# Performance work log

Hardware: AMD Instinct MI355X
Metric: run time of the kernel (lower is better)

The kernel has to match this reference:

```python
import jax, jax.numpy as jnp
import numpy as np

# ---- static configuration (mirrors qg_flux __init__ args) ----
F = 1600.0
MREFIN = 8
H1 = 0.25
NU1 = 2
NU2 = 2
NCYC = 2
M = 513
N = 513
DX = 0.001953125
DY = 0.001953125
R = 1.0
RKB = 1e-06
RKH = 1e-08
RKH2 = 2e-11
BATCH = 16
HS = [H1 / 2 ** (MREFIN - k - 1) for k in range(MREFIN)]  # grid spacing per level (0 = finest)


def _pad1(x):
    return jnp.pad(x, ((0, 0), (0, 0), (1, 1), (1, 1)))


def relax(psi, q, h):
    # Relax_Conv: 3x3 valid conv (cross stencil on psi, -1 center on q) scaled by 1/(4+F h^2), then zero-pad 1.
    c = 1.0 / (4.0 + F * h * h)
    inner = c * (psi[:, :, :-2, 1:-1] + psi[:, :, 2:, 1:-1]
                 + psi[:, :, 1:-1, :-2] + psi[:, :, 1:-1, 2:]
                 - q[:, :, 1:-1, 1:-1])
    return _pad1(inner)


def rescale(psi, q, h):
    # Rescal_Conv: 5x5 stride-2 valid conv, centers at odd-even input points, then zero-pad 1.
    d = 4.0 + F * h * h
    S, T = psi.shape[-2], psi.shape[-1]
    no = (S - 5) // 2 + 1
    mo = (T - 5) // 2 + 1
    rc = slice(2, 2 * no + 1, 2)   # center rows
    cc = slice(2, 2 * mo + 1, 2)   # center cols
    ctr = psi[:, :, rc, cc]
    up = psi[:, :, 1:2 * no:2, cc]
    dn = psi[:, :, 3:2 * no + 2:2, cc]
    lf = psi[:, :, rc, 1:2 * mo:2]
    rt = psi[:, :, rc, 3:2 * mo + 2:2]
    qc = q[:, :, rc, cc]
    out = 4.0 * (d * ctr - up - dn - lf - rt + qc)
    return _pad1(out)


def bilinear_up(x, hf, wf):
    # torch F.interpolate(mode='bilinear', align_corners=True)
    hc, wc = x.shape[-2], x.shape[-1]
    ys = jnp.linspace(0.0, hc - 1.0, hf)
    xs = jnp.linspace(0.0, wc - 1.0, wf)
    y0 = jnp.clip(jnp.floor(ys), 0, hc - 2).astype(jnp.int32)
    x0 = jnp.clip(jnp.floor(xs), 0, wc - 2).astype(jnp.int32)
    wy = (ys - y0)[:, None]
    wx = xs - x0
    row = x[:, :, y0, :] * (1.0 - wy) + x[:, :, y0 + 1, :] * wy
    return row[:, :, :, x0] * (1.0 - wx) + row[:, :, :, x0 + 1] * wx


def helmholtz(psiguess, q):
    bs, ch, w, h = psiguess.shape
    shapes = [(int(np.ceil(w / 2 ** k)), int(np.ceil(h / 2 ** k))) for k in range(MREFIN)]
    psis = [jnp.zeros((bs, ch) + s, dtype=psiguess.dtype) for s in shapes]
    qs = [jnp.zeros((bs, ch) + s, dtype=psiguess.dtype) for s in shapes]
    psis[0] = psiguess
    qs[0] = q * HS[0] ** 2
    for _ic in range(NCYC):
        # downsweep: relax fine->coarse, restrict residual-equation RHS
        for k in range(MREFIN):
            if k != 0:
                psis[k] = jnp.zeros_like(psis[k])
            for _ in range(NU1):
                psis[k] = relax(psis[k], qs[k], HS[k])
            if k < MREFIN - 1:
                qs[k + 1] = rescale(psis[k], qs[k], HS[k])
        # upsweep (faithful to original loop ordering, incl. its intadd indexing)
        for k in range(MREFIN):
            lvl = MREFIN - k - 1
            for _ in range(NU2):
                psis[lvl] = relax(psis[lvl], qs[lvl], HS[lvl])
            if k > 0:
                hf, wf = psis[k - 1].shape[-2], psis[k - 1].shape[-1]
                psis[k - 1] = psis[k - 1] + bilinear_up(psis[k], hf, wf)
    return psis[0]


def arakawa(A, B):
    # 9-point Arakawa Jacobian, zero on boundary
    Amm = A[:, :, :-2, :-2]; Am0 = A[:, :, :-2, 1:-1]; Amp = A[:, :, :-2, 2:]
    A0m = A[:, :, 1:-1, :-2];                         A0p = A[:, :, 1:-1, 2:]
    Apm = A[:, :, 2:, :-2];  Ap0 = A[:, :, 2:, 1:-1]; App = A[:, :, 2:, 2:]
    Bmm = B[:, :, :-2, :-2]; Bm0 = B[:, :, :-2, 1:-1]; Bmp = B[:, :, :-2, 2:]
    B0m = B[:, :, 1:-1, :-2];                          B0p = B[:, :, 1:-1, 2:]
    Bpm = B[:, :, 2:, :-2];  Bp0 = B[:, :, 2:, 1:-1];  Bpp = B[:, :, 2:, 2:]
    J = ((A0m - Am0) * Bmm
         + (Amm + A0m - Amp - A0p) * Bm0
         + (Am0 - A0p) * Bmp
         + (Apm + Ap0 - Amm - Am0) * B0m
         + (Am0 + Amp - Ap0 - App) * B0p
         + (Ap0 - A0m) * Bpm
         + (A0p + App - A0m - Apm) * Bp0
         + (A0p - Ap0) * Bpp)
    return _pad1(J / (12.0 * DX * DY))


def laplacian(A):
    dx2, dy2 = DX * DX, DY * DY
    inner = ((A[:, :, 1:-1, :-2] + A[:, :, 1:-1, 2:]) / dx2
             + (A[:, :, :-2, 1:-1] + A[:, :, 2:, 1:-1]) / dy2
             - A[:, :, 1:-1, 1:-1] * (2.0 / dx2 + 2.0 / dy2))
    return _pad1(inner)


def setup_inputs() -> dict:
    key = jax.random.key(0)
    k1, k2, k3 = jax.random.split(key, 3)
    PSIGUESS = 0.1 * jax.random.normal(k1, (BATCH, 1, M, N), dtype=jnp.float32)
    Q = 0.1 * jax.random.normal(k2, (BATCH, 1, M, N), dtype=jnp.float32)
    CURLT = 0.1 * jax.random.normal(k3, (1, M, N), dtype=jnp.float32)
    return {"t": 0, "PSIGUESS": PSIGUESS, "Q": Q, "CURLT": CURLT}


def reference(t, PSIGUESS, Q, CURLT):
    PSI = helmholtz(PSIGUESS, Q)
    J = arakawa(PSI, Q)
    Z = laplacian(PSI)
    Z2 = laplacian(Z)
    Z4 = laplacian(Z2)
    base = -R * J - RKB * Z + RKH * Z2 - RKH2 * Z4 + CURLT  # CURLT (1,M,N) broadcasts
    inner = base[:, :, 1:-1, 1:-1] - (0.5 / DX) * (PSI[:, :, 1:-1, 2:] - PSI[:, :, 1:-1, :-2])
    QFLUX = _pad1(inner)
    return (PSI, QFLUX)
```

## Files before the change

### kernel.cpp

```cpp
#include <hip/hip_runtime.h>


#define N0 513
#define N1 257
#define NB 16

#define C0F ((float)(1.0 / 4.006103515625))
#define D0F 4.006103515625f
#define C1F ((float)(1.0 / 4.0244140625))
#define H0SQ 3.814697265625e-06f
#define INV_DX2 262144.0f
#define CENTER  1048576.0f
#define INV12S  ((float)(262144.0 / 12.0 * 262144.0))

template<bool INT>
__device__ __forceinline__ void drelaxR_body(
    const float* __restrict__ P, const float* __restrict__ Q,
    float* __restrict__ outp, float* __restrict__ q1p,
    int ti, int tj, int ic0, int jc0, size_t base, size_t cbase, int lid,
    float* __restrict__ sIn, float* __restrict__ sQ,
    float* __restrict__ sT, float* __restrict__ sP) {
  const int n = N0;
  for (int t = lid; t < 38 * 38; t += 256) {
    int r = t / 38, c = t - r * 38;
    int gi = ti - 3 + r, gj = tj - 3 + c;
    float v;
    if constexpr (INT) v = P[(size_t)gi * n + gj];
    else v = (gi >= 0 && gi < n && gj >= 0 && gj < n) ? P[(size_t)gi * n + gj] : 0.f;
    sIn[r * 39 + c] = v;
  }
  for (int t = lid; t < 36 * 36; t += 256) {
    int r = t / 36, c = t - r * 36;
    int gi = ti - 2 + r, gj = tj - 2 + c;
    float v;
    if constexpr (INT) v = Q[(size_t)gi * n + gj] * H0SQ;
    else v = (gi >= 0 && gi < n && gj >= 0 && gj < n) ? Q[(size_t)gi * n + gj] * H0SQ : 0.f;
    sQ[r * 37 + c] = v;
  }
  __syncthreads();
  for (int t = lid; t < 36 * 36; t += 256) {
    int r = t / 36, c = t - r * 36;
    float v = 0.f;
    if (INT || ((ti - 2 + r) >= 1 && (ti - 2 + r) < n - 1 && (tj - 2 + c) >= 1 && (tj - 2 + c) < n - 1))
      v = C0F * (sIn[r * 39 + c + 1] + sIn[(r + 2) * 39 + c + 1] +
                 sIn[(r + 1) * 39 + c] + sIn[(r + 1) * 39 + c + 2] - sQ[r * 37 + c]);
    sT[r * 37 + c] = v;
  }
  __syncthreads();
  for (int t = lid; t < 34 * 34; t += 256) {
    int r = t / 34, c = t - r * 34;
    float v = 0.f;
    if (INT || ((ti - 1 + r) >= 1 && (ti - 1 + r) < n - 1 && (tj - 1 + c) >= 1 && (tj - 1 + c) < n - 1))
      v = C0F * (sT[r * 37 + c + 1] + sT[(r + 2) * 37 + c + 1] +
                 sT[(r + 1) * 37 + c] + sT[(r + 1) * 37 + c + 2] - sQ[(r + 1) * 37 + c + 1]);
    sP[r * 35 + c] = v;
  }
  __syncthreads();
  int tx = lid & 31, ty = lid >> 5;
  #pragma unroll
  for (int s = 0; s < 4; s++) {
    int yy = ty + 8 * s;
    int i = ti + yy, j = tj + tx;
    if (INT || (i < n && j < n))
      outp[base + (size_t)i * n + j] = sP[(yy + 1) * 35 + tx + 1];
  }
  {
    int cy = lid >> 4, cx = lid & 15;
    int ic = ic0 + cy, jc = jc0 + cx;
    if constexpr (INT) {
      int r = 2 * cy + 1, c = 2 * cx + 1;
      float v = 4.f * (D0F * sP[r * 35 + c] - sP[(r - 1) * 35 + c] - sP[(r + 1) * 35 + c]
                       - sP[r * 35 + c - 1] - sP[r * 35 + c + 1] + sQ[(r + 1) * 37 + c + 1]);
      q1p[cbase + (size_t)ic * N1 + jc] = v;
    } else {
      if (ic < N1 && jc < N1) {
        float v = 0.f;
        if (ic >= 1 && ic < N1 - 1 && jc >= 1 && jc < N1 - 1) {
          int r = 2 * cy + 1, c = 2 * cx + 1;
          v = 4.f * (D0F * sP[r * 35 + c] - sP[(r - 1) * 35 + c] - sP[(r + 1) * 35 + c]
                     - sP[r * 35 + c - 1] - sP[r * 35 + c + 1] + sQ[(r + 1) * 37 + c + 1]);
        }
        q1p[cbase + (size_t)ic * N1 + jc] = v;
      }
    }
  }
}

__global__ __launch_bounds__(256) void drelaxR_k(
    const float* __restrict__ psi, const float* __restrict__ Qg,
    float* __restrict__ out, float* __restrict__ q1) {
  __shared__ float smem[38 * 39 + 36 * 37 + 36 * 37];
  float* sIn = smem;
  float* sQ  = smem + 38 * 39;
  float* sT  = sQ + 36 * 37;
  float* sP  = smem;
  int bx = blockIdx.x, by = blockIdx.y;
  int ti = by * 32, tj = bx * 32;
  size_t base = (size_t)blockIdx.z * (N0 * N0);
  size_t cbase = (size_t)blockIdx.z * (N1 * N1);
  int lid = threadIdx.y * 32 + threadIdx.x;
  bool inter = (bx >= 1 && bx <= 14 && by >= 1 && by <= 14);
  if (inter)
    drelaxR_body<true>(psi + base, Qg + base, out, q1, ti, tj, 16 * by, 16 * bx,
                       base, cbase, lid, sIn, sQ, sT, sP);
  else
    drelaxR_body<false>(psi + base, Qg + base, out, q1, ti, tj, 16 * by, 16 * bx,
                        base, cbase, lid, sIn, sQ, sT, sP);
}

template<bool INT>
__device__ __forceinline__ void vleg_body(
    const float* __restrict__ P, const float* __restrict__ Q,
    const float* __restrict__ q1, float* __restrict__ outp, float* __restrict__ q1o,
    int ti, int tj, int c0i, int c0j, int ic0, int jc0,
    size_t base, size_t cbase, int lid,
    float* __restrict__ bufA, float* __restrict__ bufB,
    float* __restrict__ bufC, float* __restrict__ bufD) {
  const int n = N0;
  float* sq1 = bufD;
  float* sp1 = bufD + 25 * 26;
  for (int t = lid; t < 25 * 25; t += 256) {
    int r = t / 25, c = t - r * 25;
    int ci = c0i - 1 + r, cj = c0j - 1 + c;
    float v;
    if constexpr (INT) v = q1[(size_t)ci * N1 + cj];
    else v = (ci >= 0 && ci < N1 && cj >= 0 && cj < N1) ? q1[(size_t)ci * N1 + cj] : 0.f;
    sq1[r * 26 + c] = v;
  }
  for (int t = lid; t < 40 * 40; t += 256) {
    int r = t / 40, c = t - r * 40;
    int gi = ti - 4 + r, gj = tj - 4 + c;
    float v;
    if constexpr (INT) v = Q[(size_t)gi * n + gj] * H0SQ;
    else v = (gi >= 0 && gi < n && gj >= 0 && gj < n) ? Q[(size_t)gi * n + gj] * H0SQ : 0.f;
    bufB[r * 41 + c] = v;
  }
  __syncthreads();
  for (int t = lid; t < 23 * 23; t += 256) {
    int r = t / 23, c = t - r * 23;
    float v = 0.f;
    if (INT || ((c0i + r) >= 1 && (c0i + r) < N1 - 1 && (c0j + c) >= 1 && (c0j + c) < N1 - 1))
      v = C1F * (-C1F * (sq1[r * 26 + c + 1] + sq1[(r + 2) * 26 + c + 1] +
                         sq1[(r + 1) * 26 + c] + sq1[(r + 1) * 26 + c + 2])
                 - sq1[(r + 1) * 26 + c + 1]);
    sp1[r * 24 + c] = v;
  }
  __syncthreads();
  for (int t = lid; t < 42 * 42; t += 256) {
    int r = t / 42, c = t - r * 42;
    int gi = ti - 5 + r, gj = tj - 5 + c;
    float v = 0.f;
    if (INT || (gi >= 0 && gi < n && gj >= 0 && gj < n)) {
      int r1 = (gi >> 1) - c0i, c1 = (gj >> 1) - c0j;
      float a = sp1[r1 * 24 + c1],       b = sp1[r1 * 24 + c1 + 1];
      float e = sp1[(r1 + 1) * 24 + c1], d = sp1[(r1 + 1) * 24 + c1 + 1];
      float wx = (gj & 1) ? 0.5f : 0.f, wy = (gi & 1) ? 0.5f : 0.f;
      float r0 = a + wx * (b - a), rr = e + wx * (d - e);
      v = P[(size_t)gi * n + gj] + (r0 + wy * (rr - r0));
    }
    bufA[r * 43 + c] = v;
  }
  __syncthreads();
  for (int t = lid; t < 40 * 40; t += 256) {
    int r = t / 40, c = t - r * 40;
    float v = 0.f;
    if (INT || ((ti - 4 + r) >= 1 && (ti - 4 + r) < n - 1 && (tj - 4 + c) >= 1 && (tj - 4 + c) < n - 1))
      v = C0F * (bufA[r * 43 + c + 1] + bufA[(r + 2) * 43 + c + 1] +
                 bufA[(r + 1) * 43 + c] + bufA[(r + 1) * 43 + c + 2] - bufB[r * 41 + c]);
    bufC[r * 41 + c] = v;
  }
  __syncthreads();
  for (int t = lid; t < 38 * 38; t += 256) {
    int r = t / 38, c = t - r * 38;
    float v = 0.f;
    if (INT || ((ti - 3 + r) >= 1 && (ti - 3 + r) < n - 1 && (tj - 3 + c) >= 1 && (tj - 3 + c) < n - 1))
      v = C0F * (bufC[r * 41 + c + 1] + bufC[(r + 2) * 41 + c + 1] +
                 bufC[(r + 1) * 41 + c] + bufC[(r + 1) * 41 + c + 2] - bufB[(r + 1) * 41 + c + 1]);
    bufD[r * 39 + c] = v;
  }
  __syncthreads();
  for (int t = lid; t < 36 * 36; t += 256) {
    int r = t / 36, c = t - r * 36;
    float v = 0.f;
    if (INT || ((ti - 2 + r) >= 1 && (ti - 2 + r) < n - 1 && (tj - 2 + c) >= 1 && (tj - 2 + c) < n - 1))
      v = C0F * (bufD[r * 39 + c + 1] + bufD[(r + 2) * 39 + c + 1] +
                 bufD[(r + 1) * 39 + c] + bufD[(r + 1) * 39 + c + 2] - bufB[(r + 2) * 41 + c + 2]);
    bufA[r * 37 + c] = v;
  }
  __syncthreads();
  for (int t = lid; t < 34 * 34; t += 256) {
    int r = t / 34, c = t - r * 34;
    float v = 0.f;
    if (INT || ((ti - 1 + r) >= 1 && (ti - 1 + r) < n - 1 && (tj - 1 + c) >= 1 && (tj - 1 + c) < n - 1))
      v = C0F * (bufA[r * 37 + c + 1] + bufA[(r + 2) * 37 + c + 1] +
                 bufA[(r + 1) * 37 + c] + bufA[(r + 1) * 37 + c + 2] - bufB[(r + 3) * 41 + c + 3]);
    bufC[r * 35 + c] = v;
  }
  __syncthreads();
  int tx = lid & 31, ty = lid >> 5;
  #pragma unroll
  for (int s = 0; s < 4; s++) {
    int yy = ty + 8 * s;
    int i = ti + yy, j = tj + tx;
    if (INT || (i < n && j < n))
      outp[base + (size_t)i * n + j] = bufC[(yy + 1) * 35 + tx + 1];
  }
  {
    int cy = lid >> 4, cx = lid & 15;
    int ic = ic0 + cy, jc = jc0 + cx;
    if constexpr (INT) {
      int r = 2 * cy + 1, c = 2 * cx + 1;
      float v = 4.f * (D0F * bufC[r * 35 + c] - bufC[(r - 1) * 35 + c] - bufC[(r + 1) * 35 + c]
                       - bufC[r * 35 + c - 1] - bufC[r * 35 + c + 1]
                       + bufB[(2 * cy + 4) * 41 + 2 * cx + 4]);
      q1o[cbase + (size_t)ic * N1 + jc] = v;
    } else {
      if (ic < N1 && jc < N1) {
        float v = 0.f;
        if (ic >= 1 && ic < N1 - 1 && jc >= 1 && jc < N1 - 1) {
          int r = 2 * cy + 1, c = 2 * cx + 1;
          v = 4.f * (D0F * bufC[r * 35 + c] - bufC[(r - 1) * 35 + c] - bufC[(r + 1) * 35 + c]
                     - bufC[r * 35 + c - 1] - bufC[r * 35 + c + 1]
                     + bufB[(2 * cy + 4) * 41 + 2 * cx + 4]);
        }
        q1o[cbase + (size_t)ic * N1 + jc] = v;
      }
    }
  }
}

__global__ __launch_bounds__(256) void vleg_k(
    const float* __restrict__ psi, const float* __restrict__ Qg,
    const float* __restrict__ q1g, float* __restrict__ out, float* __restrict__ q1o) {
  __shared__ float bufA[42 * 43];
  __shared__ float bufB[40 * 41];
  __shared__ float bufC[40 * 41];
  __shared__ float bufD[38 * 39];
  int bx = blockIdx.x, by = blockIdx.y;
  int ti = by * 32, tj = bx * 32;
  int c0i = 16 * by - 3, c0j = 16 * bx - 3;
  size_t base = (size_t)blockIdx.z * (N0 * N0);
  size_t cbase = (size_t)blockIdx.z * (N1 * N1);
  const float* q1 = q1g + cbase;
  int lid = threadIdx.y * 32 + threadIdx.x;
  bool inter = (bx >= 1 && bx <= 14 && by >= 1 && by <= 14);
  if (inter)
    vleg_body<true>(psi + base, Qg + base, q1, out, q1o, ti, tj, c0i, c0j,
                    16 * by, 16 * bx, base, cbase, lid, bufA, bufB, bufC, bufD);
  else
    vleg_body<false>(psi + base, Qg + base, q1, out, q1o, ti, tj, c0i, c0j,
                     16 * by, 16 * bx, base, cbase, lid, bufA, bufB, bufC, bufD);
}

template<bool INT>
__device__ __forceinline__ void mega_body(
    const float* __restrict__ P, const float* __restrict__ Q,
    const float* __restrict__ q1, const float* __restrict__ CT,
    float* __restrict__ psi_out, float* __restrict__ qf_out,
    int ti, int tj, int c0i, int c0j, size_t base, int lid,
    float* __restrict__ bufA, float* __restrict__ bufB,
    float* __restrict__ bufC, float* __restrict__ bufD) {
  const int n = N0;
  float* sq1 = bufD;
  float* sp1 = bufD + 25 * 26;
  for (int t = lid; t < 25 * 25; t += 256) {
    int r = t / 25, c = t - r * 25;
    int ci = c0i - 1 + r, cj = c0j - 1 + c;
    float v;
    if constexpr (INT) v = q1[(size_t)ci * N1 + cj];
    else v = (ci >= 0 && ci < N1 && cj >= 0 && cj < N1) ? q1[(size_t)ci * N1 + cj] : 0.f;
    sq1[r * 26 + c] = v;
  }
  for (int t = lid; t < 40 * 40; t += 256) {
    int r = t / 40, c = t - r * 40;
    int gi = ti - 4 + r, gj = tj - 4 + c;
    float v;
    if constexpr (INT) v = Q[(size_t)gi * n + gj] * H0SQ;
    else v = (gi >= 0 && gi < n && gj >= 0 && gj < n) ? Q[(size_t)gi * n + gj] * H0SQ : 0.f;
    bufB[r * 41 + c] = v;
  }
  __syncthreads();
  for (int t = lid; t < 23 * 23; t += 256) {
    int r = t / 23, c = t - r * 23;
    float v = 0.f;
    if (INT || ((c0i + r) >= 1 && (c0i + r) < N1 - 1 && (c0j + c) >= 1 && (c0j + c) < N1 - 1))
      v = C1F * (-C1F * (sq1[r * 26 + c + 1] + sq1[(r + 2) * 26 + c + 1] +
                         sq1[(r + 1) * 26 + c] + sq1[(r + 1) * 26 + c + 2])
                 - sq1[(r + 1) * 26 + c + 1]);
    sp1[r * 24 + c] = v;
  }
  __syncthreads();
  for (int t = lid; t < 42 * 42; t += 256) {
    int r = t / 42, c = t - r * 42;
    int gi = ti - 5 + r, gj = tj - 5 + c;
    float v = 0.f;
    if (INT || (gi >= 0 && gi < n && gj >= 0 && gj < n)) {
      int r1 = (gi >> 1) - c0i, c1 = (gj >> 1) - c0j;
      float a = sp1[r1 * 24 + c1],       b = sp1[r1 * 24 + c1 + 1];
      float e = sp1[(r1 + 1) * 24 + c1], d = sp1[(r1 + 1) * 24 + c1 + 1];
      float wx = (gj & 1) ? 0.5f : 0.f, wy = (gi & 1) ? 0.5f : 0.f;
      float r0 = a + wx * (b - a), rr = e + wx * (d - e);
      v = P[(size_t)gi * n + gj] + (r0 + wy * (rr - r0));
    }
    bufA[r * 43 + c] = v;
  }
  __syncthreads();
  for (int t = lid; t < 40 * 40; t += 256) {
    int r = t / 40, c = t - r * 40;
    float v = 0.f;
    if (INT || ((ti - 4 + r) >= 1 && (ti - 4 + r) < n - 1 && (tj - 4 + c) >= 1 && (tj - 4 + c) < n - 1))
      v = C0F * (bufA[r * 43 + c + 1] + bufA[(r + 2) * 43 + c + 1] +
                 bufA[(r + 1) * 43 + c] + bufA[(r + 1) * 43 + c + 2] - bufB[r * 41 + c]);
    bufC[r * 41 + c] = v;
  }
  __syncthreads();
  for (int t = lid; t < 38 * 38; t += 256) {
    int r = t / 38, c = t - r * 38;
    float v = 0.f;
    if (INT || ((ti - 3 + r) >= 1 && (ti - 3 + r) < n - 1 && (tj - 3 + c) >= 1 && (tj - 3 + c) < n - 1))
      v = C0F * (bufC[r * 41 + c + 1] + bufC[(r + 2) * 41 + c + 1] +
                 bufC[(r + 1) * 41 + c] + bufC[(r + 1) * 41 + c + 2] - bufB[(r + 1) * 41 + c + 1]);
    bufD[r * 39 + c] = v;
  }
  __syncthreads();
  for (int t = lid; t < 36 * 36; t += 256) {
    int r = t / 36, c = t - r * 36;
    float v = 0.f;
    if (INT || ((ti - 2 + r) >= 1 && (ti - 2 + r) < n - 1 && (tj - 2 + c) >= 1 && (tj - 2 + c) < n - 1))
      v = (bufD[r * 39 + c + 1] + bufD[(r + 2) * 39 + c + 1] +
           bufD[(r + 1) * 39 + c] + bufD[(r + 1) * 39 + c + 2]) * INV_DX2
          - bufD[(r + 1) * 39 + c + 1] * CENTER;
    bufA[r * 37 + c] = v;
  }
  __syncthreads();
  for (int t = lid; t < 34 * 34; t += 256) {
    int r = t / 34, c = t - r * 34;
    float v = 0.f;
    if (INT || ((ti - 1 + r) >= 1 && (ti - 1 + r) < n - 1 && (tj - 1 + c) >= 1 && (tj - 1 + c) < n - 1))
      v = (bufA[r * 37 + c + 1] + bufA[(r + 2) * 37 + c + 1] +
           bufA[(r + 1) * 37 + c] + bufA[(r + 1) * 37 + c + 2]) * INV_DX2
          - bufA[(r + 1) * 37 + c + 1] * CENTER;
    bufC[r * 35 + c] = v;
  }
  __syncthreads();
  int tx = lid & 31, ty = lid >> 5;
  #pragma unroll
  for (int s = 0; s < 4; s++) {
    int yy = ty + 8 * s;
    int i = ti + yy, j = tj + tx;
    if (!INT && (i >= n || j >= n)) continue;
    size_t idx = base + (size_t)i * n + j;
    int pr = yy + 3, pc = tx + 3;
    psi_out[idx] = bufD[pr * 39 + pc];
    float qv = 0.f;
    if (INT || (i >= 1 && i < n - 1 && j >= 1 && j < n - 1)) {
      float z1v = bufA[(yy + 2) * 37 + tx + 2];
      int r2 = yy + 1, c2 = tx + 1;
      float z2v = bufC[r2 * 35 + c2];
      float z4 = (bufC[r2 * 35 + c2 - 1] + bufC[r2 * 35 + c2 + 1] +
                  bufC[(r2 - 1) * 35 + c2] + bufC[(r2 + 1) * 35 + c2]) * INV_DX2
                 - z2v * CENTER;
      float Amm = bufD[(pr - 1) * 39 + pc - 1], Am0 = bufD[(pr - 1) * 39 + pc],
            Amp = bufD[(pr - 1) * 39 + pc + 1];
      float A0m = bufD[pr * 39 + pc - 1], A0p = bufD[pr * 39 + pc + 1];
      float Apm = bufD[(pr + 1) * 39 + pc - 1], Ap0 = bufD[(pr + 1) * 39 + pc],
            App = bufD[(pr + 1) * 39 + pc + 1];
      int qr = yy + 4, qc = tx + 4;
      float J = (A0m - Am0) * bufB[(qr - 1) * 41 + qc - 1]
              + (Amm + A0m - Amp - A0p) * bufB[(qr - 1) * 41 + qc]
              + (Am0 - A0p) * bufB[(qr - 1) * 41 + qc + 1]
              + (Apm + Ap0 - Amm - Am0) * bufB[qr * 41 + qc - 1]
              + (Am0 + Amp - Ap0 - App) * bufB[qr * 41 + qc + 1]
              + (Ap0 - A0m) * bufB[(qr + 1) * 41 + qc - 1]
              + (A0p + App - A0m - Apm) * bufB[(qr + 1) * 41 + qc]
              + (A0p - Ap0) * bufB[(qr + 1) * 41 + qc + 1];
      J *= INV12S;
      float ct = CT[(size_t)i * n + j];
      qv = -J - 1e-6f * z1v + 1e-8f * z2v - 2e-11f * z4 + ct - 256.0f * (A0p - A0m);
    }
    qf_out[idx] = qv;
  }
}

__global__ __launch_bounds__(256) void mega_k(
    const float* __restrict__ psi, const float* __restrict__ Qg,
    const float* __restrict__ q1g, const float* __restrict__ CT,
    float* __restrict__ psi_out, float* __restrict__ qf_out) {
  __shared__ float bufA[42 * 43];
  __shared__ float bufB[40 * 41];
  __shared__ float bufC[40 * 41];
  __shared__ float bufD[38 * 39];
  int bx = blockIdx.x, by = blockIdx.y;
  int ti = by * 32, tj = bx * 32;
  int c0i = 16 * by - 3, c0j = 16 * bx - 3;
  size_t base = (size_t)blockIdx.z * (N0 * N0);
  const float* q1 = q1g + (size_t)blockIdx.z * (N1 * N1);
  int lid = threadIdx.y * 32 + threadIdx.x;
  bool inter = (bx >= 1 && bx <= 14 && by >= 1 && by <= 14);
  if (inter)
    mega_body<true>(psi + base, Qg + base, q1, CT, psi_out, qf_out,
                    ti, tj, c0i, c0j, base, lid, bufA, bufB, bufC, bufD);
  else
    mega_body<false>(psi + base, Qg + base, q1, CT, psi_out, qf_out,
                     ti, tj, c0i, c0j, base, lid, bufA, bufB, bufC, bufD);
}

extern "C" void kernel_launch(void* const* d_in, const int* in_sizes, int n_in,
                              void* d_out, int out_size, void* d_ws, size_t ws_size,
                              hipStream_t stream) {
  const float* PSIG = (const float*)d_in[1];
  const float* Q    = (const float*)d_in[2];
  const float* CT   = (const float*)d_in[3];

  float* ws = (float*)d_ws;
  size_t f0 = (size_t)NB * N0 * N0;
  size_t f1 = (size_t)NB * N1 * N1;
  float* pA  = ws;
  float* pB  = pA + f0;
  float* q1a = pB + f0;
  float* q1b = q1a + f1;

  dim3 blk(32, 8, 1), grd(17, 17, NB);

  drelaxR_k<<<grd, blk, 0, stream>>>(PSIG, Q, pA, q1a);
  vleg_k<<<grd, blk, 0, stream>>>(pA, Q, q1a, pB, q1b);
  float* psi_out = (float*)d_out;
  float* qf_out  = psi_out + f0;
  mega_k<<<grd, blk, 0, stream>>>(pB, Q, q1b, CT, psi_out, qf_out);
}
```

Before: 117.3 us.

## Fuse two Jacobi relax sweeps into one wide stencil and use 512-thread blocks

For interior tiles, two consecutive relax sweeps are merged algebraically into one 13-point stencil (relax2c), which removes an intermediate shared-memory pass and a barrier per pair of sweeps. Blocks grow from 256 to 512 threads so each loop needs fewer iterations. The shared coarse-correction prologue is moved into a helper. The larger blocks may lower occupancy, the drelax kernel no longer aliases its shared buffers, and the fused stencil reorders floating-point operations slightly.

```diff
diff --git a/kernel.cpp b/kernel.cpp
--- a/kernel.cpp
+++ b/kernel.cpp
@@ -4,6 +4,7 @@
 #define N0 513
 #define N1 257
 #define NB 16
+#define NT 512
 
 #define C0F ((float)(1.0 / 4.006103515625))
 #define D0F 4.006103515625f
@@ -12,6 +13,15 @@
 #define INV_DX2 262144.0f
 #define CENTER  1048576.0f
 #define INV12S  ((float)(262144.0 / 12.0 * 262144.0))
+
+__device__ __forceinline__ float relax2c(const float* u, int su,
+                                         const float* qq, int sq) {
+  float X = 4.f * u[0]
+          + (u[-2 * su] + u[2 * su] + u[-2] + u[2])
+          + 2.f * (u[-su - 1] + u[-su + 1] + u[su - 1] + u[su + 1])
+          - (qq[-sq] + qq[sq] + qq[-1] + qq[1]);
+  return C0F * (C0F * X - qq[0]);
+}
 
 template<bool INT>
 __device__ __forceinline__ void drelaxR_body(
@@ -21,7 +31,7 @@
     float* __restrict__ sIn, float* __restrict__ sQ,
     float* __restrict__ sT, float* __restrict__ sP) {
   const int n = N0;
-  for (int t = lid; t < 38 * 38; t += 256) {
+  for (int t = lid; t < 38 * 38; t += NT) {
     int r = t / 38, c = t - r * 38;
     int gi = ti - 3 + r, gj = tj - 3 + c;
     float v;
@@ -29,7 +39,7 @@
     else v = (gi >= 0 && gi < n && gj >= 0 && gj < n) ? P[(size_t)gi * n + gj] : 0.f;
     sIn[r * 39 + c] = v;
   }
-  for (int t = lid; t < 36 * 36; t += 256) {
+  for (int t = lid; t < 36 * 36; t += NT) {
     int r = t / 36, c = t - r * 36;
     int gi = ti - 2 + r, gj = tj - 2 + c;
     float v;
@@ -38,33 +48,42 @@
     sQ[r * 37 + c] = v;
   }
   __syncthreads();
-  for (int t = lid; t < 36 * 36; t += 256) {
-    int r = t / 36, c = t - r * 36;
-    float v = 0.f;
-    if (INT || ((ti - 2 + r) >= 1 && (ti - 2 + r) < n - 1 && (tj - 2 + c) >= 1 && (tj - 2 + c) < n - 1))
-      v = C0F * (sIn[r * 39 + c + 1] + sIn[(r + 2) * 39 + c + 1] +
-                 sIn[(r + 1) * 39 + c] + sIn[(r + 1) * 39 + c + 2] - sQ[r * 37 + c]);
-    sT[r * 37 + c] = v;
-  }
-  __syncthreads();
-  for (int t = lid; t < 34 * 34; t += 256) {
-    int r = t / 34, c = t - r * 34;
-    float v = 0.f;
-    if (INT || ((ti - 1 + r) >= 1 && (ti - 1 + r) < n - 1 && (tj - 1 + c) >= 1 && (tj - 1 + c) < n - 1))
-      v = C0F * (sT[r * 37 + c + 1] + sT[(r + 2) * 37 + c + 1] +
-                 sT[(r + 1) * 37 + c] + sT[(r + 1) * 37 + c + 2] - sQ[(r + 1) * 37 + c + 1]);
-    sP[r * 35 + c] = v;
-  }
-  __syncthreads();
+  if constexpr (INT) {
+    for (int t = lid; t < 34 * 34; t += NT) {
+      int r = t / 34, c = t - r * 34;
+      sP[r * 35 + c] = relax2c(&sIn[(r + 2) * 39 + c + 2], 39,
+                               &sQ[(r + 1) * 37 + c + 1], 37);
+    }
+    __syncthreads();
+  } else {
+    for (int t = lid; t < 36 * 36; t += NT) {
+      int r = t / 36, c = t - r * 36;
+      float v = 0.f;
+      if ((ti - 2 + r) >= 1 && (ti - 2 + r) < n - 1 && (tj - 2 + c) >= 1 && (tj - 2 + c) < n - 1)
+        v = C0F * (sIn[r * 39 + c + 1] + sIn[(r + 2) * 39 + c + 1] +
+                   sIn[(r + 1) * 39 + c] + sIn[(r + 1) * 39 + c + 2] - sQ[r * 37 + c]);
+      sT[r * 37 + c] = v;
+    }
+    __syncthreads();
+    for (int t = lid; t < 34 * 34; t += NT) {
+      int r = t / 34, c = t - r * 34;
+      float v = 0.f;
+      if ((ti - 1 + r) >= 1 && (ti - 1 + r) < n - 1 && (tj - 1 + c) >= 1 && (tj - 1 + c) < n - 1)
+        v = C0F * (sT[r * 37 + c + 1] + sT[(r + 2) * 37 + c + 1] +
+                   sT[(r + 1) * 37 + c] + sT[(r + 1) * 37 + c + 2] - sQ[(r + 1) * 37 + c + 1]);
+      sP[r * 35 + c] = v;
+    }
+    __syncthreads();
+  }
   int tx = lid & 31, ty = lid >> 5;
   #pragma unroll
-  for (int s = 0; s < 4; s++) {
-    int yy = ty + 8 * s;
+  for (int s = 0; s < 2; s++) {
+    int yy = ty + 16 * s;
     int i = ti + yy, j = tj + tx;
     if (INT || (i < n && j < n))
       outp[base + (size_t)i * n + j] = sP[(yy + 1) * 35 + tx + 1];
   }
-  {
+  if (lid < 256) {
     int cy = lid >> 4, cx = lid & 15;
     int ic = ic0 + cy, jc = jc0 + cx;
     if constexpr (INT) {
@@ -86,14 +105,10 @@
   }
 }
 
-__global__ __launch_bounds__(256) void drelaxR_k(
+__global__ __launch_bounds__(NT) void drelaxR_k(
     const float* __restrict__ psi, const float* __restrict__ Qg,
     float* __restrict__ out, float* __restrict__ q1) {
-  __shared__ float smem[38 * 39 + 36 * 37 + 36 * 37];
-  float* sIn = smem;
-  float* sQ  = smem + 38 * 39;
-  float* sT  = sQ + 36 * 37;
-  float* sP  = smem;
+  __shared__ float sIn[38 * 39], sQ[36 * 37], sT[36 * 37], sP[34 * 35];
   int bx = blockIdx.x, by = blockIdx.y;
   int ti = by * 32, tj = bx * 32;
   size_t base = (size_t)blockIdx.z * (N0 * N0);
@@ -109,17 +124,14 @@
 }
 
 template<bool INT>
-__device__ __forceinline__ void vleg_body(
+__device__ __forceinline__ void coarse_and_v(
     const float* __restrict__ P, const float* __restrict__ Q,
-    const float* __restrict__ q1, float* __restrict__ outp, float* __restrict__ q1o,
-    int ti, int tj, int c0i, int c0j, int ic0, int jc0,
-    size_t base, size_t cbase, int lid,
+    const float* __restrict__ q1,
+    int ti, int tj, int c0i, int c0j, int lid,
     float* __restrict__ bufA, float* __restrict__ bufB,
-    float* __restrict__ bufC, float* __restrict__ bufD) {
+    float* __restrict__ sq1, float* __restrict__ sp1) {
   const int n = N0;
-  float* sq1 = bufD;
-  float* sp1 = bufD + 25 * 26;
-  for (int t = lid; t < 25 * 25; t += 256) {
+  for (int t = lid; t < 25 * 25; t += NT) {
     int r = t / 25, c = t - r * 25;
     int ci = c0i - 1 + r, cj = c0j - 1 + c;
     float v;
@@ -127,7 +139,7 @@
     else v = (ci >= 0 && ci < N1 && cj >= 0 && cj < N1) ? q1[(size_t)ci * N1 + cj] : 0.f;
     sq1[r * 26 + c] = v;
   }
-  for (int t = lid; t < 40 * 40; t += 256) {
+  for (int t = lid; t < 40 * 40; t += NT) {
     int r = t / 40, c = t - r * 40;
     int gi = ti - 4 + r, gj = tj - 4 + c;
     float v;
@@ -136,7 +148,7 @@
     bufB[r * 41 + c] = v;
   }
   __syncthreads();
-  for (int t = lid; t < 23 * 23; t += 256) {
+  for (int t = lid; t < 23 * 23; t += NT) {
     int r = t / 23, c = t - r * 23;
     float v = 0.f;
     if (INT || ((c0i + r) >= 1 && (c0i + r) < N1 - 1 && (c0j + c) >= 1 && (c0j + c) < N1 - 1))
@@ -146,7 +158,7 @@
     sp1[r * 24 + c] = v;
   }
   __syncthreads();
-  for (int t = lid; t < 42 * 42; t += 256) {
+  for (int t = lid; t < 42 * 42; t += NT) {
     int r = t / 42, c = t - r * 42;
     int gi = ti - 5 + r, gj = tj - 5 + c;
     float v = 0.f;
@@ -161,51 +173,78 @@
     bufA[r * 43 + c] = v;
   }
   __syncthreads();
-  for (int t = lid; t < 40 * 40; t += 256) {
-    int r = t / 40, c = t - r * 40;
-    float v = 0.f;
-    if (INT || ((ti - 4 + r) >= 1 && (ti - 4 + r) < n - 1 && (tj - 4 + c) >= 1 && (tj - 4 + c) < n - 1))
-      v = C0F * (bufA[r * 43 + c + 1] + bufA[(r + 2) * 43 + c + 1] +
-                 bufA[(r + 1) * 43 + c] + bufA[(r + 1) * 43 + c + 2] - bufB[r * 41 + c]);
-    bufC[r * 41 + c] = v;
-  }
-  __syncthreads();
-  for (int t = lid; t < 38 * 38; t += 256) {
-    int r = t / 38, c = t - r * 38;
-    float v = 0.f;
-    if (INT || ((ti - 3 + r) >= 1 && (ti - 3 + r) < n - 1 && (tj - 3 + c) >= 1 && (tj - 3 + c) < n - 1))
-      v = C0F * (bufC[r * 41 + c + 1] + bufC[(r + 2) * 41 + c + 1] +
-                 bufC[(r + 1) * 41 + c] + bufC[(r + 1) * 41 + c + 2] - bufB[(r + 1) * 41 + c + 1]);
-    bufD[r * 39 + c] = v;
-  }
-  __syncthreads();
-  for (int t = lid; t < 36 * 36; t += 256) {
-    int r = t / 36, c = t - r * 36;
-    float v = 0.f;
-    if (INT || ((ti - 2 + r) >= 1 && (ti - 2 + r) < n - 1 && (tj - 2 + c) >= 1 && (tj - 2 + c) < n - 1))
-      v = C0F * (bufD[r * 39 + c + 1] + bufD[(r + 2) * 39 + c + 1] +
-                 bufD[(r + 1) * 39 + c] + bufD[(r + 1) * 39 + c + 2] - bufB[(r + 2) * 41 + c + 2]);
-    bufA[r * 37 + c] = v;
-  }
-  __syncthreads();
-  for (int t = lid; t < 34 * 34; t += 256) {
-    int r = t / 34, c = t - r * 34;
-    float v = 0.f;
-    if (INT || ((ti - 1 + r) >= 1 && (ti - 1 + r) < n - 1 && (tj - 1 + c) >= 1 && (tj - 1 + c) < n - 1))
-      v = C0F * (bufA[r * 37 + c + 1] + bufA[(r + 2) * 37 + c + 1] +
-                 bufA[(r + 1) * 37 + c] + bufA[(r + 1) * 37 + c + 2] - bufB[(r + 3) * 41 + c + 3]);
-    bufC[r * 35 + c] = v;
-  }
-  __syncthreads();
+}
+
+template<bool INT>
+__device__ __forceinline__ void vleg_body(
+    const float* __restrict__ P, const float* __restrict__ Q,
+    const float* __restrict__ q1, float* __restrict__ outp, float* __restrict__ q1o,
+    int ti, int tj, int c0i, int c0j, int ic0, int jc0,
+    size_t base, size_t cbase, int lid,
+    float* __restrict__ bufA, float* __restrict__ bufB,
+    float* __restrict__ bufC, float* __restrict__ bufD) {
+  const int n = N0;
+  coarse_and_v<INT>(P, Q, q1, ti, tj, c0i, c0j, lid, bufA, bufB, bufD, bufD + 25 * 26);
+  if constexpr (INT) {
+    for (int t = lid; t < 38 * 38; t += NT) {
+      int r = t / 38, c = t - r * 38;
+      bufD[r * 39 + c] = relax2c(&bufA[(r + 2) * 43 + c + 2], 43,
+                                 &bufB[(r + 1) * 41 + c + 1], 41);
+    }
+    __syncthreads();
+    for (int t = lid; t < 34 * 34; t += NT) {
+      int r = t / 34, c = t - r * 34;
+      bufC[r * 35 + c] = relax2c(&bufD[(r + 2) * 39 + c + 2], 39,
+                                 &bufB[(r + 3) * 41 + c + 3], 41);
+    }
+    __syncthreads();
+  } else {
+    for (int t = lid; t < 40 * 40; t += NT) {
+      int r = t / 40, c = t - r * 40;
+      float v = 0.f;
+      if ((ti - 4 + r) >= 1 && (ti - 4 + r) < n - 1 && (tj - 4 + c) >= 1 && (tj - 4 + c) < n - 1)
+        v = C0F * (bufA[r * 43 + c + 1] + bufA[(r + 2) * 43 + c + 1] +
+                   bufA[(r + 1) * 43 + c] + bufA[(r + 1) * 43 + c + 2] - bufB[r * 41 + c]);
+      bufC[r * 41 + c] = v;
+    }
+    __syncthreads();
+    for (int t = lid; t < 38 * 38; t += NT) {
+      int r = t / 38, c = t - r * 38;
+      float v = 0.f;
+      if ((ti - 3 + r) >= 1 && (ti - 3 + r) < n - 1 && (tj - 3 + c) >= 1 && (tj - 3 + c) < n - 1)
+        v = C0F * (bufC[r * 41 + c + 1] + bufC[(r + 2) * 41 + c + 1] +
+                   bufC[(r + 1) * 41 + c] + bufC[(r + 1) * 41 + c + 2] - bufB[(r + 1) * 41 + c + 1]);
+      bufD[r * 39 + c] = v;
+    }
+    __syncthreads();
+    for (int t = lid; t < 36 * 36; t += NT) {
+      int r = t / 36, c = t - r * 36;
+      float v = 0.f;
+      if ((ti - 2 + r) >= 1 && (ti - 2 + r) < n - 1 && (tj - 2 + c) >= 1 && (tj - 2 + c) < n - 1)
+        v = C0F * (bufD[r * 39 + c + 1] + bufD[(r + 2) * 39 + c + 1] +
+                   bufD[(r + 1) * 39 + c] + bufD[(r + 1) * 39 + c + 2] - bufB[(r + 2) * 41 + c + 2]);
+      bufA[r * 37 + c] = v;
+    }
+    __syncthreads();
+    for (int t = lid; t < 34 * 34; t += NT) {
+      int r = t / 34, c = t - r * 34;
+      float v = 0.f;
+      if ((ti - 1 + r) >= 1 && (ti - 1 + r) < n - 1 && (tj - 1 + c) >= 1 && (tj - 1 + c) < n - 1)
+        v = C0F * (bufA[r * 37 + c + 1] + bufA[(r + 2) * 37 + c + 1] +
+                   bufA[(r + 1) * 37 + c] + bufA[(r + 1) * 37 + c + 2] - bufB[(r + 3) * 41 + c + 3]);
+      bufC[r * 35 + c] = v;
+    }
+    __syncthreads();
+  }
   int tx = lid & 31, ty = lid >> 5;
   #pragma unroll
-  for (int s = 0; s < 4; s++) {
-    int yy = ty + 8 * s;
+  for (int s = 0; s < 2; s++) {
+    int yy = ty + 16 * s;
     int i = ti + yy, j = tj + tx;
     if (INT || (i < n && j < n))
       outp[base + (size_t)i * n + j] = bufC[(yy + 1) * 35 + tx + 1];
   }
-  {
+  if (lid < 256) {
     int cy = lid >> 4, cx = lid & 15;
     int ic = ic0 + cy, jc = jc0 + cx;
     if constexpr (INT) {
@@ -229,7 +268,7 @@
   }
 }
 
-__global__ __launch_bounds__(256) void vleg_k(
+__global__ __launch_bounds__(NT) void vleg_k(
     const float* __restrict__ psi, const float* __restrict__ Qg,
     const float* __restrict__ q1g, float* __restrict__ out, float* __restrict__ q1o) {
   __shared__ float bufA[42 * 43];
@@ -261,69 +300,35 @@
     float* __restrict__ bufA, float* __restrict__ bufB,
     float* __restrict__ bufC, float* __restrict__ bufD) {
   const int n = N0;
-  float* sq1 = bufD;
-  float* sp1 = bufD + 25 * 26;
-  for (int t = lid; t < 25 * 25; t += 256) {
-    int r = t / 25, c = t - r * 25;
-    int ci = c0i - 1 + r, cj = c0j - 1 + c;
-    float v;
-    if constexpr (INT) v = q1[(size_t)ci * N1 + cj];
-    else v = (ci >= 0 && ci < N1 && cj >= 0 && cj < N1) ? q1[(size_t)ci * N1 + cj] : 0.f;
-    sq1[r * 26 + c] = v;
-  }
-  for (int t = lid; t < 40 * 40; t += 256) {
-    int r = t / 40, c = t - r * 40;
-    int gi = ti - 4 + r, gj = tj - 4 + c;
-    float v;
-    if constexpr (INT) v = Q[(size_t)gi * n + gj] * H0SQ;
-    else v = (gi >= 0 && gi < n && gj >= 0 && gj < n) ? Q[(size_t)gi * n + gj] * H0SQ : 0.f;
-    bufB[r * 41 + c] = v;
-  }
-  __syncthreads();
-  for (int t = lid; t < 23 * 23; t += 256) {
-    int r = t / 23, c = t - r * 23;
-    float v = 0.f;
-    if (INT || ((c0i + r) >= 1 && (c0i + r) < N1 - 1 && (c0j + c) >= 1 && (c0j + c) < N1 - 1))
-      v = C1F * (-C1F * (sq1[r * 26 + c + 1] + sq1[(r + 2) * 26 + c + 1] +
-                         sq1[(r + 1) * 26 + c] + sq1[(r + 1) * 26 + c + 2])
-                 - sq1[(r + 1) * 26 + c + 1]);
-    sp1[r * 24 + c] = v;
-  }
-  __syncthreads();
-  for (int t = lid; t < 42 * 42; t += 256) {
-    int r = t / 42, c = t - r * 42;
-    int gi = ti - 5 + r, gj = tj - 5 + c;
-    float v = 0.f;
-    if (INT || (gi >= 0 && gi < n && gj >= 0 && gj < n)) {
-      int r1 = (gi >> 1) - c0i, c1 = (gj >> 1) - c0j;
-      float a = sp1[r1 * 24 + c1],       b = sp1[r1 * 24 + c1 + 1];
-      float e = sp1[(r1 + 1) * 24 + c1], d = sp1[(r1 + 1) * 24 + c1 + 1];
-      float wx = (gj & 1) ? 0.5f : 0.f, wy = (gi & 1) ? 0.5f : 0.f;
-      float r0 = a + wx * (b - a), rr = e + wx * (d - e);
-      v = P[(size_t)gi * n + gj] + (r0 + wy * (rr - r0));
-    }
-    bufA[r * 43 + c] = v;
-  }
-  __syncthreads();
-  for (int t = lid; t < 40 * 40; t += 256) {
-    int r = t / 40, c = t - r * 40;
-    float v = 0.f;
-    if (INT || ((ti - 4 + r) >= 1 && (ti - 4 + r) < n - 1 && (tj - 4 + c) >= 1 && (tj - 4 + c) < n - 1))
-      v = C0F * (bufA[r * 43 + c + 1] + bufA[(r + 2) * 43 + c + 1] +
-                 bufA[(r + 1) * 43 + c] + bufA[(r + 1) * 43 + c + 2] - bufB[r * 41 + c]);
-    bufC[r * 41 + c] = v;
-  }
-  __syncthreads();
-  for (int t = lid; t < 38 * 38; t += 256) {
-    int r = t / 38, c = t - r * 38;
-    float v = 0.f;
-    if (INT || ((ti - 3 + r) >= 1 && (ti - 3 + r) < n - 1 && (tj - 3 + c) >= 1 && (tj - 3 + c) < n - 1))
-      v = C0F * (bufC[r * 41 + c + 1] + bufC[(r + 2) * 41 + c + 1] +
-                 bufC[(r + 1) * 41 + c] + bufC[(r + 1) * 41 + c + 2] - bufB[(r + 1) * 41 + c + 1]);
-    bufD[r * 39 + c] = v;
-  }
-  __syncthreads();
-  for (int t = lid; t < 36 * 36; t += 256) {
+  coarse_and_v<INT>(P, Q, q1, ti, tj, c0i, c0j, lid, bufA, bufB, bufD, bufD + 25 * 26);
+  if constexpr (INT) {
+    for (int t = lid; t < 38 * 38; t += NT) {
+      int r = t / 38, c = t - r * 38;
+      bufD[r * 39 + c] = relax2c(&bufA[(r + 2) * 43 + c + 2], 43,
+                                 &bufB[(r + 1) * 41 + c + 1], 41);
+    }
+    __syncthreads();
+  } else {
+    for (int t = lid; t < 40 * 40; t += NT) {
+      int r = t / 40, c = t - r * 40;
+      float v = 0.f;
+      if ((ti - 4 + r) >= 1 && (ti - 4 + r) < n - 1 && (tj - 4 + c) >= 1 && (tj - 4 + c) < n - 1)
+        v = C0F * (bufA[r * 43 + c + 1] + bufA[(r + 2) * 43 + c + 1] +
+                   bufA[(r + 1) * 43 + c] + bufA[(r + 1) * 43 + c + 2] - bufB[r * 41 + c]);
+      bufC[r * 41 + c] = v;
+    }
+    __syncthreads();
+    for (int t = lid; t < 38 * 38; t += NT) {
+      int r = t / 38, c = t - r * 38;
+      float v = 0.f;
+      if ((ti - 3 + r) >= 1 && (ti - 3 + r) < n - 1 && (tj - 3 + c) >= 1 && (tj - 3 + c) < n - 1)
+        v = C0F * (bufC[r * 41 + c + 1] + bufC[(r + 2) * 41 + c + 1] +
+                   bufC[(r + 1) * 41 + c] + bufC[(r + 1) * 41 + c + 2] - bufB[(r + 1) * 41 + c + 1]);
+      bufD[r * 39 + c] = v;
+    }
+    __syncthreads();
+  }
+  for (int t = lid; t < 36 * 36; t += NT) {
     int r = t / 36, c = t - r * 36;
     float v = 0.f;
     if (INT || ((ti - 2 + r) >= 1 && (ti - 2 + r) < n - 1 && (tj - 2 + c) >= 1 && (tj - 2 + c) < n - 1))
@@ -333,7 +338,7 @@
     bufA[r * 37 + c] = v;
   }
   __syncthreads();
-  for (int t = lid; t < 34 * 34; t += 256) {
+  for (int t = lid; t < 34 * 34; t += NT) {
     int r = t / 34, c = t - r * 34;
     float v = 0.f;
     if (INT || ((ti - 1 + r) >= 1 && (ti - 1 + r) < n - 1 && (tj - 1 + c) >= 1 && (tj - 1 + c) < n - 1))
@@ -345,8 +350,8 @@
   __syncthreads();
   int tx = lid & 31, ty = lid >> 5;
   #pragma unroll
-  for (int s = 0; s < 4; s++) {
-    int yy = ty + 8 * s;
+  for (int s = 0; s < 2; s++) {
+    int yy = ty + 16 * s;
     int i = ti + yy, j = tj + tx;
     if (!INT && (i >= n || j >= n)) continue;
     size_t idx = base + (size_t)i * n + j;
@@ -382,7 +387,7 @@
   }
 }
 
-__global__ __launch_bounds__(256) void mega_k(
+__global__ __launch_bounds__(NT) void mega_k(
     const float* __restrict__ psi, const float* __restrict__ Qg,
     const float* __restrict__ q1g, const float* __restrict__ CT,
     float* __restrict__ psi_out, float* __restrict__ qf_out) {
@@ -420,7 +425,7 @@
   float* q1a = pB + f0;
   float* q1b = q1a + f1;
 
-  dim3 blk(32, 8, 1), grd(17, 17, NB);
+  dim3 blk(32, 16, 1), grd(17, 17, NB);
 
   drelaxR_k<<<grd, blk, 0, stream>>>(PSIG, Q, pA, q1a);
   vleg_k<<<grd, blk, 0, stream>>>(pA, Q, q1a, pB, q1b);
```

New measurement: 110.8 us. 1.06x faster.
